# Kernel tuning notes

Measured on AMD Instinct MI355X. Metric: run time of the kernel, lower is better.

Reference implementation:

```python
import jax, jax.numpy as jnp
import numpy as np

TEMP = 0.07
EPS_NORM = 1e-12  # torch F.normalize clamp eps
EPS_RENORM = 1e-9


def _l2_normalize(x):
    n = jnp.linalg.norm(x, axis=1, keepdims=True)
    return x / jnp.maximum(n, EPS_NORM)


def setup_inputs() -> dict:
    key = jax.random.key(0)
    k1, k2 = jax.random.split(key)
    feat = jax.random.normal(k1, (65536, 1024), dtype=jnp.float32)
    prompts = jax.random.normal(k2, (1000, 1024), dtype=jnp.float32) * 0.01
    return {"feat": feat, "prompts": prompts, "topk": 2}


def reference(feat, prompts, topk):
    # cosine similarity between normalized feat and normalized prompts
    p_n = _l2_normalize(prompts)            # [C, d]
    q_n = _l2_normalize(feat)               # [N, d]
    sims = jnp.matmul(q_n, p_n.T)           # [N, C]
    probs = jax.nn.softmax(sims / TEMP, axis=1)
    num_classes = prompts.shape[0]
    if topk is not None and topk < num_classes:
        _, topk_idx = jax.lax.top_k(probs, topk)          # [N, k]
        rows = jnp.arange(probs.shape[0])[:, None]        # [N, 1]
        mask = jnp.zeros_like(probs).at[rows, topk_idx].set(1.0)
        probs = probs * mask
        probs = probs / (jnp.sum(probs, axis=1, keepdims=True) + EPS_RENORM)
    mixed_prompt = jnp.matmul(probs, prompts)             # [N, d]
    return (mixed_prompt, probs)
```

## Files before the change

kernel.cpp:

```cpp
#include <hip/hip_runtime.h>
#include <cstdint>

using f32x4 = __attribute__((ext_vector_type(4))) float;
using s16x8 = __attribute__((ext_vector_type(8))) short;
typedef unsigned short u16;

typedef const __attribute__((address_space(1))) uint32_t* gptr_t;
typedef __attribute__((address_space(3))) uint32_t* lptr_t;

__device__ __forceinline__ u16 f2bf(float f) {
  union { float f; uint32_t u; } v; v.f = f;
  uint32_t r = v.u + 0x7FFFu + ((v.u >> 16) & 1u);
  return (u16)(r >> 16);
}
__device__ __forceinline__ float bf2f(u16 b) {
  union { uint32_t u; float f; } v; v.u = ((uint32_t)b) << 16;
  return v.f;
}

__global__ __launch_bounds__(256) void k_prep_prompts(const float* __restrict__ prompts,
                                                      u16* __restrict__ p_bf) {
  const int r = blockIdx.x;
  const int t = threadIdx.x;
  if (r >= 1000) {
    if (t < 128) {
      s16x8 z = {0, 0, 0, 0, 0, 0, 0, 0};
      ((s16x8*)(p_bf + (size_t)r * 1024))[t] = z;
    }
    return;
  }
  float4 x = ((const float4*)(prompts + (size_t)r * 1024))[t];
  float ss = x.x * x.x + x.y * x.y + x.z * x.z + x.w * x.w;
  #pragma unroll
  for (int off = 32; off; off >>= 1) ss += __shfl_xor(ss, off);
  __shared__ float red[4];
  if ((t & 63) == 0) red[t >> 6] = ss;
  __syncthreads();
  float n = fmaxf(sqrtf(red[0] + red[1] + red[2] + red[3]), 1e-12f);
  float inv = 1.0f / n;
  u16* pb = p_bf + (size_t)r * 1024 + t * 4;
  pb[0] = f2bf(x.x * inv); pb[1] = f2bf(x.y * inv);
  pb[2] = f2bf(x.z * inv); pb[3] = f2bf(x.w * inv);
}

__global__ __launch_bounds__(256) void k_feat(const float* __restrict__ feat,
                                              u16* __restrict__ out) {
  const size_t stride = (size_t)gridDim.x * 256;
  const size_t n4 = 67108864ull / 4;
  for (size_t j = (size_t)blockIdx.x * 256 + threadIdx.x; j < n4; j += stride) {
    float4 x = ((const float4*)feat)[j];
    ushort4 o;
    o.x = f2bf(x.x); o.y = f2bf(x.y); o.z = f2bf(x.z); o.w = f2bf(x.w);
    ((ushort4*)out)[j] = o;
  }
}

__global__ __launch_bounds__(256) void k_sims(const u16* __restrict__ A,
                                              const u16* __restrict__ B,
                                              u16* __restrict__ C) {
  __shared__ u16 As[2][128 * 32];
  __shared__ u16 Bs[2][128 * 32];
  const int bid = blockIdx.x;
  const int lg = (bid & 7) * 512 + (bid >> 3);
  const int bn = lg & 7;
  const int bm = lg >> 3;
  const int t = threadIdx.x;
  const int w = t >> 6, l = t & 63;
  const int wm = (w >> 1) * 64, wn = (w & 1) * 64;
  const int lrow = l & 15, lko = l >> 4;

  f32x4 zero4 = {0.f, 0.f, 0.f, 0.f};
  f32x4 acc[4][4];
  #pragma unroll
  for (int i = 0; i < 4; i++)
    #pragma unroll
    for (int j = 0; j < 4; j++) acc[i][j] = zero4;

  const int srow = t >> 2;
  const int scol = (t & 3) * 8;
  const u16* gA = A + (size_t)(bm * 128 + srow) * 1024 + scol;
  const u16* gB = B + (size_t)(bn * 128 + srow) * 1024 + scol;

  #pragma unroll
  for (int i = 0; i < 2; i++) {
    __builtin_amdgcn_global_load_lds((gptr_t)(gA + (size_t)i * 64 * 1024),
                                     (lptr_t)&As[0][(i * 64 + srow) * 32 + scol], 16, 0, 0);
    __builtin_amdgcn_global_load_lds((gptr_t)(gB + (size_t)i * 64 * 1024),
                                     (lptr_t)&Bs[0][(i * 64 + srow) * 32 + scol], 16, 0, 0);
  }
  __syncthreads();

  for (int kt = 0; kt < 32; ++kt) {
    const int cur = kt & 1;
    if (kt < 31) {
      const int nk = (kt + 1) * 32;
      #pragma unroll
      for (int i = 0; i < 2; i++) {
        __builtin_amdgcn_global_load_lds((gptr_t)(gA + (size_t)i * 64 * 1024 + nk),
                                         (lptr_t)&As[cur ^ 1][(i * 64 + srow) * 32 + scol], 16, 0, 0);
        __builtin_amdgcn_global_load_lds((gptr_t)(gB + (size_t)i * 64 * 1024 + nk),
                                         (lptr_t)&Bs[cur ^ 1][(i * 64 + srow) * 32 + scol], 16, 0, 0);
      }
    }
    s16x8 a[4], b[4];
    #pragma unroll
    for (int mi = 0; mi < 4; mi++) a[mi] = *(const s16x8*)&As[cur][(wm + mi * 16 + lrow) * 32 + lko * 8];
    #pragma unroll
    for (int ni = 0; ni < 4; ni++) b[ni] = *(const s16x8*)&Bs[cur][(wn + ni * 16 + lrow) * 32 + lko * 8];
    #pragma unroll
    for (int mi = 0; mi < 4; mi++)
      #pragma unroll
      for (int ni = 0; ni < 4; ni++)
        acc[mi][ni] = __builtin_amdgcn_mfma_f32_16x16x32_bf16(a[mi], b[ni], acc[mi][ni], 0, 0, 0);
    __syncthreads();
  }
  const int rbase = (l >> 4) * 4;
  #pragma unroll
  for (int mi = 0; mi < 4; mi++)
    #pragma unroll
    for (int ni = 0; ni < 4; ni++) {
      int gcol = bn * 128 + wn + ni * 16 + lrow;
      if (gcol >= 1000) continue;
      #pragma unroll
      for (int j = 0; j < 4; j++) {
        int grow = bm * 128 + wm + mi * 16 + rbase + j;
        C[(size_t)grow * 1000 + gcol] = f2bf(acc[mi][ni][j]);
      }
    }
}

__global__ __launch_bounds__(256) void k_topk(const float* __restrict__ feat,
                                              const float* __restrict__ prompts,
                                              const u16* __restrict__ sims,
                                              int2* __restrict__ resc,
                                              float2* __restrict__ resw) {
  const int l = threadIdx.x & 63;
  const int row = blockIdx.x * 4 + (threadIdx.x >> 6);
  const u16* srow = sims + (size_t)row * 1000;
  const float NEG = -3.0e38f;
  float s[16];
  #pragma unroll
  for (int j = 0; j < 8; j++) {
    int c = 2 * l + 128 * j;
    if (c + 1 < 1000) {
      uint32_t v = *(const uint32_t*)(srow + c);
      s[2 * j] = bf2f((u16)(v & 0xFFFFu));
      s[2 * j + 1] = bf2f((u16)(v >> 16));
    } else {
      s[2 * j] = (c < 1000) ? bf2f(srow[c]) : NEG;
      s[2 * j + 1] = NEG;
    }
  }
  const int base = l * 16;
  float q[16];
  const float4* fr = (const float4*)(feat + (size_t)row * 1024 + base);
  #pragma unroll
  for (int g = 0; g < 4; g++) {
    float4 x = fr[g];
    q[g * 4 + 0] = x.x; q[g * 4 + 1] = x.y; q[g * 4 + 2] = x.z; q[g * 4 + 3] = x.w;
  }
  float a1 = NEG, a2 = NEG;
  #pragma unroll
  for (int j = 0; j < 16; j++) {
    float v = s[j];
    bool g1 = v > a1;
    a2 = g1 ? a1 : fmaxf(a2, v);
    a1 = g1 ? v : a1;
  }
  #pragma unroll
  for (int off = 32; off; off >>= 1) {
    float b1 = __shfl_xor(a1, off), b2 = __shfl_xor(a2, off);
    float m1 = fmaxf(a1, b1);
    float m2 = fmaxf(fminf(a1, b1), fmaxf(a2, b2));
    a1 = m1; a2 = m2;
  }
  const float T = a2 - 0.25f;
  uint32_t mask = 0;
  #pragma unroll
  for (int j = 0; j < 16; j++) {
    int c = 2 * l + 128 * (j >> 1) + (j & 1);
    if (c < 1000 && s[j] >= T) mask |= (1u << j);
  }
  float qq = 0.f;
  #pragma unroll
  for (int e = 0; e < 16; e++) qq += q[e] * q[e];
  #pragma unroll
  for (int off = 32; off; off >>= 1) qq += __shfl_xor(qq, off);
  float rn = 1.0f / fmaxf(sqrtf(qq), 1e-12f);
  float s1 = NEG, s2 = NEG;
  int c1 = 0x40000000, c2 = 0x40000000;
  while (true) {
    unsigned long long act = __ballot(mask != 0);
    if (!act) break;
    int ln = (int)__ffsll(act) - 1;
    int fj = __ffs(mask) - 1;
    int myc = 2 * l + 128 * ((fj >> 1) & 7) + (fj & 1);
    int bc = __shfl(myc, ln);
    if (l == ln) mask &= (mask - 1);
    bc = (bc < 1000) ? bc : 999;
    const float4* pr = (const float4*)(prompts + (size_t)bc * 1024 + base);
    float d = 0.f, nn = 0.f;
    #pragma unroll
    for (int g = 0; g < 4; g++) {
      float4 x = pr[g];
      d += q[g * 4 + 0] * x.x; d += q[g * 4 + 1] * x.y;
      d += q[g * 4 + 2] * x.z; d += q[g * 4 + 3] * x.w;
      nn += x.x * x.x + x.y * x.y + x.z * x.z + x.w * x.w;
    }
    #pragma unroll
    for (int off = 32; off; off >>= 1) {
      d += __shfl_xor(d, off);
      nn += __shfl_xor(nn, off);
    }
    float sc = d * rn / fmaxf(sqrtf(nn), 1e-12f);
    bool b1w = (sc > s1) || (sc == s1 && bc < c1);
    bool b2w = (sc > s2) || (sc == s2 && bc < c2);
    if (b1w) { s2 = s1; c2 = c1; s1 = sc; c1 = bc; }
    else if (b2w) { s2 = sc; c2 = bc; }
  }
  float e = expf(fminf(s2 - s1, 0.0f) * (1.0f / 0.07f));
  float w1 = 1.0f / (1.0f + e);
  float w2 = e / (1.0f + e);
  if (l == 0) {
    resc[row] = make_int2(c1, c2);
    resw[row] = make_float2(w1, w2);
  }
}

__global__ __launch_bounds__(256) void k_out(const float* __restrict__ prompts,
                                             const int2* __restrict__ resc,
                                             const float2* __restrict__ resw,
                                             float* __restrict__ mixed,
                                             float* __restrict__ probs) {
  const int row = blockIdx.x;
  const int t = threadIdx.x;
  int2 cc = resc[row];
  float2 ww = resw[row];
  float4 a = ((const float4*)(prompts + (size_t)cc.x * 1024))[t];
  float4 b = ((const float4*)(prompts + (size_t)cc.y * 1024))[t];
  float4 o;
  o.x = ww.x * a.x + ww.y * b.x;
  o.y = ww.x * a.y + ww.y * b.y;
  o.z = ww.x * a.z + ww.y * b.z;
  o.w = ww.x * a.w + ww.y * b.w;
  ((float4*)(mixed + (size_t)row * 1024))[t] = o;
  if (t < 250) {
    const int base = t * 4;
    float4 z;
    z.x = (base + 0 == cc.x) ? ww.x : ((base + 0 == cc.y) ? ww.y : 0.0f);
    z.y = (base + 1 == cc.x) ? ww.x : ((base + 1 == cc.y) ? ww.y : 0.0f);
    z.z = (base + 2 == cc.x) ? ww.x : ((base + 2 == cc.y) ? ww.y : 0.0f);
    z.w = (base + 3 == cc.x) ? ww.x : ((base + 3 == cc.y) ? ww.y : 0.0f);
    ((float4*)(probs + (size_t)row * 1000))[t] = z;
  }
}

extern "C" void kernel_launch(void* const* d_in, const int* in_sizes, int n_in,
                              void* d_out, int out_size, void* d_ws, size_t ws_size,
                              hipStream_t stream) {
  int fi = 0, pi = 1;
  for (int i = 0; i < n_in; i++) {
    if (in_sizes[i] == 67108864) fi = i;
    else if (in_sizes[i] == 1024000) pi = i;
  }
  const float* feat = (const float*)d_in[fi];
  const float* prompts = (const float*)d_in[pi];

  float* mixed = (float*)d_out;
  float* probs = mixed + 67108864ull;

  u16* p_bf = (u16*)d_ws;
  int2* resc = (int2*)((char*)d_ws + (2ull << 20));
  float2* resw = (float2*)((char*)d_ws + (2ull << 20) + (512ull << 10));

  u16* feat_bf = (u16*)mixed;
  const bool big_ws = ws_size >= (1ull << 27);
  u16* sims = big_ws ? (u16*)((char*)d_ws + (3ull << 20)) : (u16*)probs;

  hipLaunchKernelGGL(k_prep_prompts, dim3(1024), dim3(256), 0, stream, prompts, p_bf);
  hipLaunchKernelGGL(k_feat, dim3(2048), dim3(256), 0, stream, feat, feat_bf);
  hipLaunchKernelGGL(k_sims, dim3(4096), dim3(256), 0, stream, feat_bf, p_bf, sims);
  hipLaunchKernelGGL(k_topk, dim3(16384), dim3(256), 0, stream, feat, prompts, sims, resc, resw);
  hipLaunchKernelGGL(k_out, dim3(65536), dim3(256), 0, stream, prompts, resc, resw, mixed, probs);
}
```

Before: 610.2 us.

## Process two rows per wave in top-k and write probs there

```diff
diff --git a/kernel.cpp b/kernel.cpp
--- a/kernel.cpp
+++ b/kernel.cpp
@@ -133,105 +133,167 @@
                                               const float* __restrict__ prompts,
                                               const u16* __restrict__ sims,
                                               int2* __restrict__ resc,
-                                              float2* __restrict__ resw) {
+                                              float2* __restrict__ resw,
+                                              float* __restrict__ probs) {
   const int l = threadIdx.x & 63;
-  const int row = blockIdx.x * 4 + (threadIdx.x >> 6);
-  const u16* srow = sims + (size_t)row * 1000;
+  const int wid = threadIdx.x >> 6;
+  const int rowA = blockIdx.x * 8 + wid * 2;
+  const int rowB = rowA + 1;
   const float NEG = -3.0e38f;
-  float s[16];
+  const u16* srA = sims + (size_t)rowA * 1000;
+  const u16* srB = sims + (size_t)rowB * 1000;
+  float sA[16], sB[16];
   #pragma unroll
   for (int j = 0; j < 8; j++) {
     int c = 2 * l + 128 * j;
     if (c + 1 < 1000) {
-      uint32_t v = *(const uint32_t*)(srow + c);
-      s[2 * j] = bf2f((u16)(v & 0xFFFFu));
-      s[2 * j + 1] = bf2f((u16)(v >> 16));
+      uint32_t vA = *(const uint32_t*)(srA + c);
+      uint32_t vB = *(const uint32_t*)(srB + c);
+      sA[2 * j] = bf2f((u16)(vA & 0xFFFFu)); sA[2 * j + 1] = bf2f((u16)(vA >> 16));
+      sB[2 * j] = bf2f((u16)(vB & 0xFFFFu)); sB[2 * j + 1] = bf2f((u16)(vB >> 16));
     } else {
-      s[2 * j] = (c < 1000) ? bf2f(srow[c]) : NEG;
-      s[2 * j + 1] = NEG;
-    }
-  }
-  const int base = l * 16;
-  float q[16];
-  const float4* fr = (const float4*)(feat + (size_t)row * 1024 + base);
-  #pragma unroll
-  for (int g = 0; g < 4; g++) {
-    float4 x = fr[g];
-    q[g * 4 + 0] = x.x; q[g * 4 + 1] = x.y; q[g * 4 + 2] = x.z; q[g * 4 + 3] = x.w;
-  }
-  float a1 = NEG, a2 = NEG;
+      sA[2 * j] = (c < 1000) ? bf2f(srA[c]) : NEG; sA[2 * j + 1] = NEG;
+      sB[2 * j] = (c < 1000) ? bf2f(srB[c]) : NEG; sB[2 * j + 1] = NEG;
+    }
+  }
+  float a1A = NEG, a2A = NEG, a1B = NEG, a2B = NEG;
   #pragma unroll
   for (int j = 0; j < 16; j++) {
-    float v = s[j];
-    bool g1 = v > a1;
-    a2 = g1 ? a1 : fmaxf(a2, v);
-    a1 = g1 ? v : a1;
+    float vA = sA[j], vB = sB[j];
+    bool gA = vA > a1A;
+    a2A = gA ? a1A : fmaxf(a2A, vA); a1A = gA ? vA : a1A;
+    bool gB = vB > a1B;
+    a2B = gB ? a1B : fmaxf(a2B, vB); a1B = gB ? vB : a1B;
   }
   #pragma unroll
   for (int off = 32; off; off >>= 1) {
-    float b1 = __shfl_xor(a1, off), b2 = __shfl_xor(a2, off);
-    float m1 = fmaxf(a1, b1);
-    float m2 = fmaxf(fminf(a1, b1), fmaxf(a2, b2));
-    a1 = m1; a2 = m2;
-  }
-  const float T = a2 - 0.25f;
-  uint32_t mask = 0;
+    float b1 = __shfl_xor(a1A, off), b2 = __shfl_xor(a2A, off);
+    float m1 = fmaxf(a1A, b1), m2 = fmaxf(fminf(a1A, b1), fmaxf(a2A, b2));
+    a1A = m1; a2A = m2;
+    float d1 = __shfl_xor(a1B, off), d2 = __shfl_xor(a2B, off);
+    float n1 = fmaxf(a1B, d1), n2 = fmaxf(fminf(a1B, d1), fmaxf(a2B, d2));
+    a1B = n1; a2B = n2;
+  }
+  const float TA = a2A - 0.25f, TB = a2B - 0.25f;
+  uint32_t maskA = 0, maskB = 0;
   #pragma unroll
   for (int j = 0; j < 16; j++) {
     int c = 2 * l + 128 * (j >> 1) + (j & 1);
-    if (c < 1000 && s[j] >= T) mask |= (1u << j);
-  }
-  float qq = 0.f;
-  #pragma unroll
-  for (int e = 0; e < 16; e++) qq += q[e] * q[e];
-  #pragma unroll
-  for (int off = 32; off; off >>= 1) qq += __shfl_xor(qq, off);
-  float rn = 1.0f / fmaxf(sqrtf(qq), 1e-12f);
-  float s1 = NEG, s2 = NEG;
-  int c1 = 0x40000000, c2 = 0x40000000;
+    if (c < 1000) {
+      if (sA[j] >= TA) maskA |= (1u << j);
+      if (sB[j] >= TB) maskB |= (1u << j);
+    }
+  }
+  const int base = l * 16;
+  float qA[16], qB[16];
+  const float4* frA = (const float4*)(feat + (size_t)rowA * 1024 + base);
+  const float4* frB = (const float4*)(feat + (size_t)rowB * 1024 + base);
+  #pragma unroll
+  for (int g = 0; g < 4; g++) {
+    float4 x = frA[g], y = frB[g];
+    qA[g * 4 + 0] = x.x; qA[g * 4 + 1] = x.y; qA[g * 4 + 2] = x.z; qA[g * 4 + 3] = x.w;
+    qB[g * 4 + 0] = y.x; qB[g * 4 + 1] = y.y; qB[g * 4 + 2] = y.z; qB[g * 4 + 3] = y.w;
+  }
+  float qqA = 0.f, qqB = 0.f;
+  #pragma unroll
+  for (int e = 0; e < 16; e++) { qqA += qA[e] * qA[e]; qqB += qB[e] * qB[e]; }
+  #pragma unroll
+  for (int off = 32; off; off >>= 1) {
+    qqA += __shfl_xor(qqA, off);
+    qqB += __shfl_xor(qqB, off);
+  }
+  float rnA = 1.0f / fmaxf(sqrtf(qqA), 1e-12f);
+  float rnB = 1.0f / fmaxf(sqrtf(qqB), 1e-12f);
+  float s1A = NEG, s2A = NEG, s1B = NEG, s2B = NEG;
+  int c1A = 0x40000000, c2A = 0x40000000, c1B = 0x40000000, c2B = 0x40000000;
   while (true) {
-    unsigned long long act = __ballot(mask != 0);
-    if (!act) break;
-    int ln = (int)__ffsll(act) - 1;
-    int fj = __ffs(mask) - 1;
-    int myc = 2 * l + 128 * ((fj >> 1) & 7) + (fj & 1);
-    int bc = __shfl(myc, ln);
-    if (l == ln) mask &= (mask - 1);
-    bc = (bc < 1000) ? bc : 999;
-    const float4* pr = (const float4*)(prompts + (size_t)bc * 1024 + base);
-    float d = 0.f, nn = 0.f;
-    #pragma unroll
-    for (int g = 0; g < 4; g++) {
-      float4 x = pr[g];
-      d += q[g * 4 + 0] * x.x; d += q[g * 4 + 1] * x.y;
-      d += q[g * 4 + 2] * x.z; d += q[g * 4 + 3] * x.w;
-      nn += x.x * x.x + x.y * x.y + x.z * x.z + x.w * x.w;
+    unsigned long long actA = __ballot(maskA != 0);
+    unsigned long long actB = __ballot(maskB != 0);
+    if (!actA && !actB) break;
+    int bcA = -1, bcB = -1;
+    if (actA) {
+      int ln = (int)__ffsll(actA) - 1;
+      int fj = __ffs(maskA) - 1;
+      int myc = 2 * l + 128 * ((fj >> 1) & 7) + (fj & 1);
+      bcA = __shfl(myc, ln);
+      if (l == ln) maskA &= (maskA - 1);
+      bcA = (bcA < 1000) ? bcA : 999;
+    }
+    if (actB) {
+      int ln = (int)__ffsll(actB) - 1;
+      int fj = __ffs(maskB) - 1;
+      int myc = 2 * l + 128 * ((fj >> 1) & 7) + (fj & 1);
+      bcB = __shfl(myc, ln);
+      if (l == ln) maskB &= (maskB - 1);
+      bcB = (bcB < 1000) ? bcB : 999;
+    }
+    float dA = 0.f, nnA = 0.f, dB = 0.f, nnB = 0.f;
+    if (bcA >= 0) {
+      const float4* pr = (const float4*)(prompts + (size_t)bcA * 1024 + base);
+      #pragma unroll
+      for (int g = 0; g < 4; g++) {
+        float4 x = pr[g];
+        dA += qA[g * 4 + 0] * x.x; dA += qA[g * 4 + 1] * x.y;
+        dA += qA[g * 4 + 2] * x.z; dA += qA[g * 4 + 3] * x.w;
+        nnA += x.x * x.x + x.y * x.y + x.z * x.z + x.w * x.w;
+      }
+    }
+    if (bcB >= 0) {
+      const float4* pr = (const float4*)(prompts + (size_t)bcB * 1024 + base);
+      #pragma unroll
+      for (int g = 0; g < 4; g++) {
+        float4 x = pr[g];
+        dB += qB[g * 4 + 0] * x.x; dB += qB[g * 4 + 1] * x.y;
+        dB += qB[g * 4 + 2] * x.z; dB += qB[g * 4 + 3] * x.w;
+        nnB += x.x * x.x + x.y * x.y + x.z * x.z + x.w * x.w;
+      }
     }
     #pragma unroll
     for (int off = 32; off; off >>= 1) {
-      d += __shfl_xor(d, off);
-      nn += __shfl_xor(nn, off);
-    }
-    float sc = d * rn / fmaxf(sqrtf(nn), 1e-12f);
-    bool b1w = (sc > s1) || (sc == s1 && bc < c1);
-    bool b2w = (sc > s2) || (sc == s2 && bc < c2);
-    if (b1w) { s2 = s1; c2 = c1; s1 = sc; c1 = bc; }
-    else if (b2w) { s2 = sc; c2 = bc; }
-  }
-  float e = expf(fminf(s2 - s1, 0.0f) * (1.0f / 0.07f));
-  float w1 = 1.0f / (1.0f + e);
-  float w2 = e / (1.0f + e);
+      dA += __shfl_xor(dA, off);  nnA += __shfl_xor(nnA, off);
+      dB += __shfl_xor(dB, off);  nnB += __shfl_xor(nnB, off);
+    }
+    if (bcA >= 0) {
+      float sc = dA * rnA / fmaxf(sqrtf(nnA), 1e-12f);
+      bool b1 = (sc > s1A) || (sc == s1A && bcA < c1A);
+      bool b2 = (sc > s2A) || (sc == s2A && bcA < c2A);
+      if (b1) { s2A = s1A; c2A = c1A; s1A = sc; c1A = bcA; }
+      else if (b2) { s2A = sc; c2A = bcA; }
+    }
+    if (bcB >= 0) {
+      float sc = dB * rnB / fmaxf(sqrtf(nnB), 1e-12f);
+      bool b1 = (sc > s1B) || (sc == s1B && bcB < c1B);
+      bool b2 = (sc > s2B) || (sc == s2B && bcB < c2B);
+      if (b1) { s2B = s1B; c2B = c1B; s1B = sc; c1B = bcB; }
+      else if (b2) { s2B = sc; c2B = bcB; }
+    }
+  }
+  float eA = expf(fminf(s2A - s1A, 0.0f) * (1.0f / 0.07f));
+  float w1A = 1.0f / (1.0f + eA), w2A = eA / (1.0f + eA);
+  float eB = expf(fminf(s2B - s1B, 0.0f) * (1.0f / 0.07f));
+  float w1B = 1.0f / (1.0f + eB), w2B = eB / (1.0f + eB);
+  float* prA = probs + (size_t)rowA * 1000;
+  float* prB = probs + (size_t)rowB * 1000;
+  #pragma unroll
+  for (int j = 0; j < 16; j++) {
+    int c = l + 64 * j;
+    if (c < 1000) {
+      prA[c] = (c == c1A) ? w1A : ((c == c2A) ? w2A : 0.0f);
+      prB[c] = (c == c1B) ? w1B : ((c == c2B) ? w2B : 0.0f);
+    }
+  }
   if (l == 0) {
-    resc[row] = make_int2(c1, c2);
-    resw[row] = make_float2(w1, w2);
-  }
-}
-
-__global__ __launch_bounds__(256) void k_out(const float* __restrict__ prompts,
-                                             const int2* __restrict__ resc,
-                                             const float2* __restrict__ resw,
-                                             float* __restrict__ mixed,
-                                             float* __restrict__ probs) {
+    resc[rowA] = make_int2(c1A, c2A);
+    resw[rowA] = make_float2(w1A, w2A);
+    resc[rowB] = make_int2(c1B, c2B);
+    resw[rowB] = make_float2(w1B, w2B);
+  }
+}
+
+__global__ __launch_bounds__(256) void k_write2(const float* __restrict__ prompts,
+                                                const int2* __restrict__ resc,
+                                                const float2* __restrict__ resw,
+                                                float* __restrict__ mixed) {
   const int row = blockIdx.x;
   const int t = threadIdx.x;
   int2 cc = resc[row];
@@ -244,15 +306,6 @@
   o.z = ww.x * a.z + ww.y * b.z;
   o.w = ww.x * a.w + ww.y * b.w;
   ((float4*)(mixed + (size_t)row * 1024))[t] = o;
-  if (t < 250) {
-    const int base = t * 4;
-    float4 z;
-    z.x = (base + 0 == cc.x) ? ww.x : ((base + 0 == cc.y) ? ww.y : 0.0f);
-    z.y = (base + 1 == cc.x) ? ww.x : ((base + 1 == cc.y) ? ww.y : 0.0f);
-    z.z = (base + 2 == cc.x) ? ww.x : ((base + 2 == cc.y) ? ww.y : 0.0f);
-    z.w = (base + 3 == cc.x) ? ww.x : ((base + 3 == cc.y) ? ww.y : 0.0f);
-    ((float4*)(probs + (size_t)row * 1000))[t] = z;
-  }
 }
 
 extern "C" void kernel_launch(void* const* d_in, const int* in_sizes, int n_in,
@@ -273,13 +326,12 @@
   int2* resc = (int2*)((char*)d_ws + (2ull << 20));
   float2* resw = (float2*)((char*)d_ws + (2ull << 20) + (512ull << 10));
 
-  u16* feat_bf = (u16*)mixed;
-  const bool big_ws = ws_size >= (1ull << 27);
-  u16* sims = big_ws ? (u16*)((char*)d_ws + (3ull << 20)) : (u16*)probs;
+  u16* sims = (u16*)mixed;
+  u16* feat_bf = (u16*)probs;
 
   hipLaunchKernelGGL(k_prep_prompts, dim3(1024), dim3(256), 0, stream, prompts, p_bf);
   hipLaunchKernelGGL(k_feat, dim3(2048), dim3(256), 0, stream, feat, feat_bf);
   hipLaunchKernelGGL(k_sims, dim3(4096), dim3(256), 0, stream, feat_bf, p_bf, sims);
-  hipLaunchKernelGGL(k_topk, dim3(16384), dim3(256), 0, stream, feat, prompts, sims, resc, resw);
-  hipLaunchKernelGGL(k_out, dim3(65536), dim3(256), 0, stream, prompts, resc, resw, mixed, probs);
-}
+  hipLaunchKernelGGL(k_topk, dim3(8192), dim3(256), 0, stream, feat, prompts, sims, resc, resw, probs);
+  hipLaunchKernelGGL(k_write2, dim3(65536), dim3(256), 0, stream, prompts, resc, resw, mixed);
+}
```

After: 573.0 us. -6.1%, faster.

## Split top-k into screening and rescoring kernels, write probs during rescore

Applied to the files above, without the earlier changes.

```diff
diff --git a/kernel.cpp b/kernel.cpp
--- a/kernel.cpp
+++ b/kernel.cpp
@@ -129,11 +129,8 @@
     }
 }
 
-__global__ __launch_bounds__(256) void k_topk(const float* __restrict__ feat,
-                                              const float* __restrict__ prompts,
-                                              const u16* __restrict__ sims,
-                                              int2* __restrict__ resc,
-                                              float2* __restrict__ resw) {
+__global__ __launch_bounds__(256) void k_screen(const u16* __restrict__ sims,
+                                                u16* __restrict__ cand) {
   const int l = threadIdx.x & 63;
   const int row = blockIdx.x * 4 + (threadIdx.x >> 6);
   const u16* srow = sims + (size_t)row * 1000;
@@ -151,14 +148,6 @@
       s[2 * j + 1] = NEG;
     }
   }
-  const int base = l * 16;
-  float q[16];
-  const float4* fr = (const float4*)(feat + (size_t)row * 1024 + base);
-  #pragma unroll
-  for (int g = 0; g < 4; g++) {
-    float4 x = fr[g];
-    q[g * 4 + 0] = x.x; q[g * 4 + 1] = x.y; q[g * 4 + 2] = x.z; q[g * 4 + 3] = x.w;
-  }
   float a1 = NEG, a2 = NEG;
   #pragma unroll
   for (int j = 0; j < 16; j++) {
@@ -181,15 +170,10 @@
     int c = 2 * l + 128 * (j >> 1) + (j & 1);
     if (c < 1000 && s[j] >= T) mask |= (1u << j);
   }
-  float qq = 0.f;
-  #pragma unroll
-  for (int e = 0; e < 16; e++) qq += q[e] * q[e];
-  #pragma unroll
-  for (int off = 32; off; off >>= 1) qq += __shfl_xor(qq, off);
-  float rn = 1.0f / fmaxf(sqrtf(qq), 1e-12f);
-  float s1 = NEG, s2 = NEG;
-  int c1 = 0x40000000, c2 = 0x40000000;
-  while (true) {
+  u16* crow = cand + (size_t)row * 16;
+  if (l < 16) crow[l] = 0xFFFFu;
+  #pragma unroll 1
+  for (int it = 0; it < 16; ++it) {
     unsigned long long act = __ballot(mask != 0);
     if (!act) break;
     int ln = (int)__ffsll(act) - 1;
@@ -197,41 +181,152 @@
     int myc = 2 * l + 128 * ((fj >> 1) & 7) + (fj & 1);
     int bc = __shfl(myc, ln);
     if (l == ln) mask &= (mask - 1);
-    bc = (bc < 1000) ? bc : 999;
-    const float4* pr = (const float4*)(prompts + (size_t)bc * 1024 + base);
-    float d = 0.f, nn = 0.f;
-    #pragma unroll
-    for (int g = 0; g < 4; g++) {
-      float4 x = pr[g];
-      d += q[g * 4 + 0] * x.x; d += q[g * 4 + 1] * x.y;
-      d += q[g * 4 + 2] * x.z; d += q[g * 4 + 3] * x.w;
-      nn += x.x * x.x + x.y * x.y + x.z * x.z + x.w * x.w;
+    if (l == 0) crow[it] = (u16)(bc < 1000 ? bc : 999);
+  }
+  if (__ballot(mask != 0) && l == 0) crow[15] = 0xFFFEu;
+}
+
+__global__ __launch_bounds__(256) void k_rescore(const float* __restrict__ feat,
+                                                 const float* __restrict__ prompts,
+                                                 const u16* __restrict__ cand,
+                                                 const u16* __restrict__ sims,
+                                                 int2* __restrict__ resc,
+                                                 float2* __restrict__ resw,
+                                                 float* __restrict__ probs) {
+  const int l = threadIdx.x & 63;
+  const int row = blockIdx.x * 4 + (threadIdx.x >> 6);
+  const float NEG = -3.0e38f;
+  int myc = (int)cand[(size_t)row * 16 + (l & 15)];
+  const bool ovf = (__shfl(myc, 15) == 0xFFFE);
+  const int base = l * 16;
+  float q[16];
+  const float4* fr = (const float4*)(feat + (size_t)row * 1024 + base);
+  #pragma unroll
+  for (int g = 0; g < 4; g++) {
+    float4 x = fr[g];
+    q[g * 4 + 0] = x.x; q[g * 4 + 1] = x.y; q[g * 4 + 2] = x.z; q[g * 4 + 3] = x.w;
+  }
+  float qq = 0.f;
+  #pragma unroll
+  for (int e = 0; e < 16; e++) qq += q[e] * q[e];
+  #pragma unroll
+  for (int off = 32; off; off >>= 1) qq += __shfl_xor(qq, off);
+  float rn = 1.0f / fmaxf(sqrtf(qq), 1e-12f);
+
+  float s1 = NEG, s2 = NEG;
+  int c1 = 0x40000000, c2 = 0x40000000;
+  if (!ovf) {
+    const int cnt = __popcll(__ballot(myc != 0xFFFF) & 0xFFFFull);
+    #pragma unroll 1
+    for (int i = 0; i < cnt; ++i) {
+      int bc = __shfl(myc, i);
+      bc = (bc < 1000) ? bc : 999;
+      const float4* pr = (const float4*)(prompts + (size_t)bc * 1024 + base);
+      float d = 0.f, nn = 0.f;
+      #pragma unroll
+      for (int g = 0; g < 4; g++) {
+        float4 x = pr[g];
+        d += q[g * 4 + 0] * x.x; d += q[g * 4 + 1] * x.y;
+        d += q[g * 4 + 2] * x.z; d += q[g * 4 + 3] * x.w;
+        nn += x.x * x.x + x.y * x.y + x.z * x.z + x.w * x.w;
+      }
+      #pragma unroll
+      for (int off = 32; off; off >>= 1) {
+        d += __shfl_xor(d, off);
+        nn += __shfl_xor(nn, off);
+      }
+      float sc = d * rn / fmaxf(sqrtf(nn), 1e-12f);
+      bool b1 = (sc > s1) || (sc == s1 && bc < c1);
+      bool b2 = (sc > s2) || (sc == s2 && bc < c2);
+      if (b1) { s2 = s1; c2 = c1; s1 = sc; c1 = bc; }
+      else if (b2) { s2 = sc; c2 = bc; }
+    }
+  } else {
+    const u16* srow = sims + (size_t)row * 1000;
+    float s[16];
+    #pragma unroll
+    for (int j = 0; j < 8; j++) {
+      int c = 2 * l + 128 * j;
+      if (c + 1 < 1000) {
+        uint32_t v = *(const uint32_t*)(srow + c);
+        s[2 * j] = bf2f((u16)(v & 0xFFFFu));
+        s[2 * j + 1] = bf2f((u16)(v >> 16));
+      } else {
+        s[2 * j] = (c < 1000) ? bf2f(srow[c]) : NEG;
+        s[2 * j + 1] = NEG;
+      }
+    }
+    float a1 = NEG, a2 = NEG;
+    #pragma unroll
+    for (int j = 0; j < 16; j++) {
+      float v = s[j];
+      bool g1 = v > a1;
+      a2 = g1 ? a1 : fmaxf(a2, v);
+      a1 = g1 ? v : a1;
     }
     #pragma unroll
     for (int off = 32; off; off >>= 1) {
-      d += __shfl_xor(d, off);
-      nn += __shfl_xor(nn, off);
-    }
-    float sc = d * rn / fmaxf(sqrtf(nn), 1e-12f);
-    bool b1w = (sc > s1) || (sc == s1 && bc < c1);
-    bool b2w = (sc > s2) || (sc == s2 && bc < c2);
-    if (b1w) { s2 = s1; c2 = c1; s1 = sc; c1 = bc; }
-    else if (b2w) { s2 = sc; c2 = bc; }
+      float b1 = __shfl_xor(a1, off), b2 = __shfl_xor(a2, off);
+      float m1 = fmaxf(a1, b1);
+      float m2 = fmaxf(fminf(a1, b1), fmaxf(a2, b2));
+      a1 = m1; a2 = m2;
+    }
+    const float T = a2 - 0.25f;
+    uint32_t mask = 0;
+    #pragma unroll
+    for (int j = 0; j < 16; j++) {
+      int c = 2 * l + 128 * (j >> 1) + (j & 1);
+      if (c < 1000 && s[j] >= T) mask |= (1u << j);
+    }
+    while (true) {
+      unsigned long long act = __ballot(mask != 0);
+      if (!act) break;
+      int ln = (int)__ffsll(act) - 1;
+      int fj = __ffs(mask) - 1;
+      int mc = 2 * l + 128 * ((fj >> 1) & 7) + (fj & 1);
+      int bc = __shfl(mc, ln);
+      if (l == ln) mask &= (mask - 1);
+      bc = (bc < 1000) ? bc : 999;
+      const float4* pr = (const float4*)(prompts + (size_t)bc * 1024 + base);
+      float d = 0.f, nn = 0.f;
+      #pragma unroll
+      for (int g = 0; g < 4; g++) {
+        float4 x = pr[g];
+        d += q[g * 4 + 0] * x.x; d += q[g * 4 + 1] * x.y;
+        d += q[g * 4 + 2] * x.z; d += q[g * 4 + 3] * x.w;
+        nn += x.x * x.x + x.y * x.y + x.z * x.z + x.w * x.w;
+      }
+      #pragma unroll
+      for (int off = 32; off; off >>= 1) {
+        d += __shfl_xor(d, off);
+        nn += __shfl_xor(nn, off);
+      }
+      float sc = d * rn / fmaxf(sqrtf(nn), 1e-12f);
+      bool b1 = (sc > s1) || (sc == s1 && bc < c1);
+      bool b2 = (sc > s2) || (sc == s2 && bc < c2);
+      if (b1) { s2 = s1; c2 = c1; s1 = sc; c1 = bc; }
+      else if (b2) { s2 = sc; c2 = bc; }
+    }
   }
   float e = expf(fminf(s2 - s1, 0.0f) * (1.0f / 0.07f));
   float w1 = 1.0f / (1.0f + e);
   float w2 = e / (1.0f + e);
+  float* prow = probs + (size_t)row * 1000;
+  #pragma unroll
+  for (int j = 0; j < 16; j++) {
+    int c = l + 64 * j;
+    if (c < 1000) prow[c] = (c == c1) ? w1 : ((c == c2) ? w2 : 0.0f);
+  }
   if (l == 0) {
     resc[row] = make_int2(c1, c2);
     resw[row] = make_float2(w1, w2);
   }
 }
 
-__global__ __launch_bounds__(256) void k_out(const float* __restrict__ prompts,
-                                             const int2* __restrict__ resc,
-                                             const float2* __restrict__ resw,
-                                             float* __restrict__ mixed,
-                                             float* __restrict__ probs) {
+__global__ __launch_bounds__(256) void k_write2(const float* __restrict__ prompts,
+                                                const int2* __restrict__ resc,
+                                                const float2* __restrict__ resw,
+                                                float* __restrict__ mixed) {
   const int row = blockIdx.x;
   const int t = threadIdx.x;
   int2 cc = resc[row];
@@ -244,15 +339,6 @@
   o.z = ww.x * a.z + ww.y * b.z;
   o.w = ww.x * a.w + ww.y * b.w;
   ((float4*)(mixed + (size_t)row * 1024))[t] = o;
-  if (t < 250) {
-    const int base = t * 4;
-    float4 z;
-    z.x = (base + 0 == cc.x) ? ww.x : ((base + 0 == cc.y) ? ww.y : 0.0f);
-    z.y = (base + 1 == cc.x) ? ww.x : ((base + 1 == cc.y) ? ww.y : 0.0f);
-    z.z = (base + 2 == cc.x) ? ww.x : ((base + 2 == cc.y) ? ww.y : 0.0f);
-    z.w = (base + 3 == cc.x) ? ww.x : ((base + 3 == cc.y) ? ww.y : 0.0f);
-    ((float4*)(probs + (size_t)row * 1000))[t] = z;
-  }
 }
 
 extern "C" void kernel_launch(void* const* d_in, const int* in_sizes, int n_in,
@@ -272,14 +358,16 @@
   u16* p_bf = (u16*)d_ws;
   int2* resc = (int2*)((char*)d_ws + (2ull << 20));
   float2* resw = (float2*)((char*)d_ws + (2ull << 20) + (512ull << 10));
-
-  u16* feat_bf = (u16*)mixed;
-  const bool big_ws = ws_size >= (1ull << 27);
-  u16* sims = big_ws ? (u16*)((char*)d_ws + (3ull << 20)) : (u16*)probs;
+  u16* cand = (u16*)((char*)d_ws + (3ull << 20));
+
+  u16* sims = (u16*)mixed;
+  u16* feat_bf = (u16*)probs;
 
   hipLaunchKernelGGL(k_prep_prompts, dim3(1024), dim3(256), 0, stream, prompts, p_bf);
   hipLaunchKernelGGL(k_feat, dim3(2048), dim3(256), 0, stream, feat, feat_bf);
   hipLaunchKernelGGL(k_sims, dim3(4096), dim3(256), 0, stream, feat_bf, p_bf, sims);
-  hipLaunchKernelGGL(k_topk, dim3(16384), dim3(256), 0, stream, feat, prompts, sims, resc, resw);
-  hipLaunchKernelGGL(k_out, dim3(65536), dim3(256), 0, stream, prompts, resc, resw, mixed, probs);
-}
+  hipLaunchKernelGGL(k_screen, dim3(16384), dim3(256), 0, stream, sims, cand);
+  hipLaunchKernelGGL(k_rescore, dim3(16384), dim3(256), 0, stream,
+                     feat, prompts, cand, sims, resc, resw, probs);
+  hipLaunchKernelGGL(k_write2, dim3(65536), dim3(256), 0, stream, prompts, resc, resw, mixed);
+}
```

Result: faster. 575.5 us (-5.7%).
